# Performance work log

Hardware: AMD Instinct MI355X
Metric: run time of the kernel (lower is better)

## Reference

```python
import jax, jax.numpy as jnp
import numpy as np

N_NODES = 50000
N_EDGES = 800000
NFEAT = 128
NHID = 128
NCLASS = 10
N_GRAPHS = 256


def _segment_mean(vals, idx, num):
    # scatter-mean: sum then divide by count, count clamped to 1 (PyG 'mean' semantics)
    s = jax.ops.segment_sum(vals, idx, num_segments=num)
    c = jax.ops.segment_sum(jnp.ones((vals.shape[0], 1), vals.dtype), idx, num_segments=num)
    return s / jnp.maximum(c, 1.0)


def _graph_conv(x, src, dst, W_n, b_n, W_s):
    # gather x at source nodes, scatter-mean into destination nodes
    agg = _segment_mean(x[src], dst, x.shape[0])          # [N, C_in]
    return agg @ W_n.T + b_n + x @ W_s.T                  # [N, C_out]


def setup_inputs() -> dict:
    key = jax.random.key(0)
    ks = jax.random.split(key, 12)

    def lin_w(k, o, i):
        return (jax.random.uniform(k, (o, i), jnp.float32) * 2.0 - 1.0) / np.sqrt(i)

    x = jax.random.normal(ks[0], (N_NODES, NFEAT), jnp.float32)
    edge_index = jax.random.randint(ks[1], (2, N_EDGES), 0, N_NODES, dtype=jnp.int32)
    batch = jnp.sort(jax.random.randint(ks[2], (N_NODES,), 0, N_GRAPHS, dtype=jnp.int32))

    return {
        "x": x,
        "edge_index": edge_index,
        "batch": batch,
        "W1n": lin_w(ks[3], NHID, NFEAT), "b1": jnp.zeros((NHID,), jnp.float32), "W1s": lin_w(ks[4], NHID, NFEAT),
        "W2n": lin_w(ks[5], NHID, NHID), "b2": jnp.zeros((NHID,), jnp.float32), "W2s": lin_w(ks[6], NHID, NHID),
        "W3n": lin_w(ks[7], NHID, NHID), "b3": jnp.zeros((NHID,), jnp.float32), "W3s": lin_w(ks[8], NHID, NHID),
        "Wlin": lin_w(ks[9], NCLASS, NHID), "blin": jnp.zeros((NCLASS,), jnp.float32),
    }


def reference(x, edge_index, batch, W1n, b1, W1s, W2n, b2, W2s, W3n, b3, W3s, Wlin, blin):
    src, dst = edge_index[0], edge_index[1]
    h = jax.nn.relu(_graph_conv(x, src, dst, W1n, b1, W1s))
    h = jax.nn.relu(_graph_conv(h, src, dst, W2n, b2, W2s))
    h = jax.nn.relu(_graph_conv(h, src, dst, W3n, b3, W3s))
    g = _segment_mean(h, batch, N_GRAPHS)                 # global_mean_pool -> [G, NHID]
    # dropout is identity at inference
    logits = g @ Wlin.T + blin                            # [G, NCLASS]
    return jax.nn.log_softmax(logits, axis=1)
```

## Files before the change

kernel.cpp:

```cpp
#include <hip/hip_runtime.h>
#include <hip/hip_bf16.h>

#define NNODES 50000
#define NEDGES 800000
#define NFEAT 128
#define NHID 128
#define NCLASS 10
#define NGRAPHS 256

#define NB 391
#define HB 512

typedef __attribute__((ext_vector_type(8))) short short8;
typedef __attribute__((ext_vector_type(4))) short short4v;
typedef __attribute__((ext_vector_type(4))) float floatx4;

__device__ __forceinline__ float bf2f(unsigned short u) {
    union { unsigned i; float f; } c; c.i = ((unsigned)u) << 16; return c.f;
}
__device__ __forceinline__ unsigned short f2bf(float f) {
    union { float f; unsigned i; } c; c.f = f;
    unsigned x = c.i;
    unsigned r = (x + 0x7fffu + ((x >> 16) & 1u)) >> 16;
    return (unsigned short)r;
}
__device__ __forceinline__ float blo(unsigned v) { return bf2f((unsigned short)(v & 0xffffu)); }
__device__ __forceinline__ float bhi(unsigned v) { return bf2f((unsigned short)(v >> 16)); }

__device__ __forceinline__ void gload_lds16(const void* gsrc, void* ldst) {
    __builtin_amdgcn_global_load_lds(
        (const __attribute__((address_space(1))) void*)gsrc,
        (__attribute__((address_space(3))) void*)ldst, 16, 0, 0);
}

__global__ __launch_bounds__(256) void k_hist(const int* __restrict__ dst,
                                              int* __restrict__ hist) {
    __shared__ int lh[NB];
    int tid = threadIdx.x;
    for (int b = tid; b < NB; b += 256) lh[b] = 0;
    __syncthreads();
    for (int i = blockIdx.x * 256 + tid; i < NEDGES; i += HB * 256)
        atomicAdd(&lh[dst[i] >> 7], 1);
    __syncthreads();
    for (int b = tid; b < NB; b += 256) hist[b * HB + blockIdx.x] = lh[b];
}

__global__ __launch_bounds__(256) void k_scanA(const int* __restrict__ hist,
                                               int* __restrict__ base,
                                               int* __restrict__ tot) {
    int q = blockIdx.x;
    int tid = threadIdx.x;
    int w = tid >> 6, l = tid & 63;
    int v0 = hist[q * HB + 2 * tid];
    int v1 = hist[q * HB + 2 * tid + 1];
    int s = v0 + v1;
    int ps = s;
    #pragma unroll
    for (int d = 1; d < 64; d <<= 1) { int y = __shfl_up(ps, d); if (l >= d) ps += y; }
    __shared__ int wsum[4];
    if (l == 63) wsum[w] = ps;
    __syncthreads();
    int wbase = 0;
    #pragma unroll
    for (int k = 0; k < 4; ++k) wbase += (k < w) ? wsum[k] : 0;
    int excl = wbase + ps - s;
    base[q * HB + 2 * tid] = excl;
    base[q * HB + 2 * tid + 1] = excl + v0;
    if (tid == 255) tot[q] = wbase + ps;
}

__global__ __launch_bounds__(512) void k_scanB(const int* __restrict__ tot,
                                               int* __restrict__ boff,
                                               int* __restrict__ row_ptr,
                                               const int* __restrict__ batch,
                                               int* __restrict__ gstart) {
    int tid = threadIdx.x;
    int wid = tid >> 6, l = tid & 63;
    if (tid <= NGRAPHS) {
        int lo = 0, hi = NNODES;
        while (lo < hi) { int mid = (lo + hi) >> 1; if (batch[mid] < tid) lo = mid + 1; else hi = mid; }
        gstart[tid] = lo;
    }
    if (wid == 0) {
        int carry = 0;
        #pragma unroll
        for (int c = 0; c < (NB + 63) / 64; ++c) {
            int i = c * 64 + l;
            int v = (i < NB) ? tot[i] : 0;
            int s = v;
            #pragma unroll
            for (int d = 1; d < 64; d <<= 1) { int y = __shfl_up(s, d); if (l >= d) s += y; }
            if (i < NB) boff[i] = carry + s - v;
            carry += __shfl(s, 63);
        }
        if (l == 0) { boff[NB] = carry; row_ptr[NNODES] = carry; }
    }
}

__global__ __launch_bounds__(256) void k_scatter(const int* __restrict__ src,
                                                 const int* __restrict__ dst,
                                                 const int* __restrict__ base,
                                                 const int* __restrict__ boff,
                                                 unsigned* __restrict__ ebuf) {
    __shared__ int cur[NB];
    int tid = threadIdx.x;
    for (int b = tid; b < NB; b += 256) cur[b] = boff[b] + base[b * HB + blockIdx.x];
    __syncthreads();
    for (int i = blockIdx.x * 256 + tid; i < NEDGES; i += HB * 256) {
        int d = dst[i];
        int bin = d >> 7;
        int pos = atomicAdd(&cur[bin], 1);
        ebuf[pos] = (unsigned)src[i] | ((unsigned)(d & 127) << 16);
    }
}

__global__ __launch_bounds__(256) void k_bcsr(const unsigned* __restrict__ ebuf,
                                              const int* __restrict__ boff,
                                              int* __restrict__ row_ptr,
                                              unsigned short* __restrict__ esrc) {
    __shared__ int deg[128];
    __shared__ int curs[128];
    int tid = threadIdx.x;
    int b = blockIdx.x;
    int s = boff[b], e = boff[b + 1];
    if (tid < 128) deg[tid] = 0;
    __syncthreads();
    for (int i = s + tid; i < e; i += 256) atomicAdd(&deg[ebuf[i] >> 16], 1);
    __syncthreads();
    if (tid == 0) {
        int run = s;
        for (int i = 0; i < 128; ++i) { curs[i] = run; run += deg[i]; }
    }
    __syncthreads();
    if (tid < 128) {
        int node = b * 128 + tid;
        if (node < NNODES) row_ptr[node] = curs[tid];
    }
    __syncthreads();
    for (int i = s + tid; i < e; i += 256) {
        unsigned pk = ebuf[i];
        int pos = atomicAdd(&curs[pk >> 16], 1);
        esrc[pos] = (unsigned short)(pk & 0xffffu);
    }
}

__global__ void k_cvt(const float* __restrict__ x,
                      const float* __restrict__ w0, const float* __restrict__ w1,
                      const float* __restrict__ w2, const float* __restrict__ w3,
                      const float* __restrict__ w4, const float* __restrict__ w5,
                      unsigned short* __restrict__ xb, unsigned short* __restrict__ wb) {
    int gid = blockIdx.x * blockDim.x + threadIdx.x;
    const int NX4 = NNODES * NFEAT / 4;
    const floatx4* srcv;
    short4v* dstv;
    if (gid < NX4) {
        srcv = (const floatx4*)x + gid;
        dstv = (short4v*)xb + gid;
    } else {
        int j = gid - NX4;
        if (j >= 6 * 4096) return;
        int m = j >> 12;
        int o4 = j & 4095;
        const float* w = (m == 0) ? w0 : (m == 1) ? w1 : (m == 2) ? w2
                       : (m == 3) ? w3 : (m == 4) ? w4 : w5;
        srcv = (const floatx4*)w + o4;
        dstv = (short4v*)wb + (m * 4096 + o4);
    }
    floatx4 v = *srcv;
    short4v o;
    #pragma unroll
    for (int k = 0; k < 4; ++k) o[k] = (short)f2bf(v[k]);
    *dstv = o;
}

__global__ __launch_bounds__(512, 6) void k_layer(const unsigned short* __restrict__ feat,
                                                  const int* __restrict__ row_ptr,
                                                  const unsigned short* __restrict__ esrc,
                                                  const unsigned short* __restrict__ Bn,
                                                  const unsigned short* __restrict__ Bs,
                                                  const float* __restrict__ bias,
                                                  unsigned short* __restrict__ out) {
    __shared__ __align__(16) unsigned short ldsA[2][8192];
    int w = threadIdx.x >> 6;
    int l = threadIdx.x & 63;
    int r = l & 15;
    int gk = l >> 4;
    int m0 = blockIdx.x * 64;

    {
        int c = l & 15;
        #pragma unroll
        for (int is = 0; is < 2; ++is) {
            int row = is * 32 + (w << 2) + (l >> 4);
            int nrow = m0 + row; if (nrow >= NNODES) nrow = NNODES - 1;
            gload_lds16(feat + (size_t)nrow * 128 + ((c ^ (row & 15)) << 3),
                        &ldsA[1][(is * 32 + (w << 2)) * 128]);
        }
    }

    const unsigned* feat32 = (const unsigned*)feat;
    unsigned* A1 = (unsigned*)&ldsA[0][0];
    #pragma unroll 1
    for (int i = 0; i < 8; ++i) {
        int row = (w << 3) + i;
        int n = m0 + row;
        float a0 = 0.f, a1 = 0.f;
        int nb = 0;
        if (n < NNODES) {
            int beg = row_ptr[n];
            nb = row_ptr[n + 1] - beg;
            for (int base = 0; base < nb; base += 64) {
                int rem = nb - base;
                int cnt = rem < 64 ? rem : 64;
                int myidx = (l < cnt) ? (int)esrc[beg + base + l] : 0;
                int j = 0;
                for (; j + 8 <= cnt; j += 8) {
                    int s0 = __shfl(myidx, j);
                    int s1 = __shfl(myidx, j + 1);
                    int s2 = __shfl(myidx, j + 2);
                    int s3 = __shfl(myidx, j + 3);
                    int s4 = __shfl(myidx, j + 4);
                    int s5 = __shfl(myidx, j + 5);
                    int s6 = __shfl(myidx, j + 6);
                    int s7 = __shfl(myidx, j + 7);
                    unsigned v0 = feat32[s0 * 64 + l];
                    unsigned v1 = feat32[s1 * 64 + l];
                    unsigned v2 = feat32[s2 * 64 + l];
                    unsigned v3 = feat32[s3 * 64 + l];
                    unsigned v4 = feat32[s4 * 64 + l];
                    unsigned v5 = feat32[s5 * 64 + l];
                    unsigned v6 = feat32[s6 * 64 + l];
                    unsigned v7 = feat32[s7 * 64 + l];
                    a0 += ((blo(v0) + blo(v1)) + (blo(v2) + blo(v3)))
                        + ((blo(v4) + blo(v5)) + (blo(v6) + blo(v7)));
                    a1 += ((bhi(v0) + bhi(v1)) + (bhi(v2) + bhi(v3)))
                        + ((bhi(v4) + bhi(v5)) + (bhi(v6) + bhi(v7)));
                }
                for (; j + 4 <= cnt; j += 4) {
                    int s0 = __shfl(myidx, j);
                    int s1 = __shfl(myidx, j + 1);
                    int s2 = __shfl(myidx, j + 2);
                    int s3 = __shfl(myidx, j + 3);
                    unsigned v0 = feat32[s0 * 64 + l];
                    unsigned v1 = feat32[s1 * 64 + l];
                    unsigned v2 = feat32[s2 * 64 + l];
                    unsigned v3 = feat32[s3 * 64 + l];
                    a0 += (blo(v0) + blo(v1)) + (blo(v2) + blo(v3));
                    a1 += (bhi(v0) + bhi(v1)) + (bhi(v2) + bhi(v3));
                }
                for (; j < cnt; ++j) {
                    int s0 = __shfl(myidx, j);
                    unsigned v0 = feat32[s0 * 64 + l];
                    a0 += blo(v0);
                    a1 += bhi(v0);
                }
            }
        }
        float inv = 1.0f / (float)max(nb, 1);
        unsigned o = ((unsigned)f2bf(a0 * inv)) | (((unsigned)f2bf(a1 * inv)) << 16);
        int c = l >> 2;
        A1[row * 64 + ((c ^ (row & 15)) << 2) + (l & 3)] = o;
    }

    short8 bf[8];
    #pragma unroll
    for (int kt = 0; kt < 8; ++kt) {
        const unsigned short* Bbase = (kt < 4 ? Bn : Bs);
        bf[kt] = *(const short8*)(Bbase + (w * 16 + r) * 128 + (kt & 3) * 32 + gk * 8);
    }
    int o = w * 16 + r;
    float bias_v = bias[o];

    __syncthreads();

    #pragma unroll
    for (int t = 0; t < 4; ++t) {
        floatx4 acc = {0.f, 0.f, 0.f, 0.f};
        #pragma unroll
        for (int half = 0; half < 2; ++half) {
            short8 af[4];
            #pragma unroll
            for (int kk = 0; kk < 4; ++kk) {
                int Cr = (((kk << 2) + gk) ^ r) << 3;
                af[kk] = *(const short8*)(&ldsA[half][(t * 16 + r) * 128 + Cr]);
            }
            #pragma unroll
            for (int kk = 0; kk < 4; ++kk)
                acc = __builtin_amdgcn_mfma_f32_16x16x32_bf16(af[kk], bf[half * 4 + kk], acc, 0, 0, 0);
        }
        #pragma unroll
        for (int j = 0; j < 4; ++j) {
            int mrow = m0 + t * 16 + gk * 4 + j;
            if (mrow < NNODES) {
                float v = acc[j] + bias_v;
                v = v > 0.f ? v : 0.f;
                out[mrow * 128 + o] = f2bf(v);
            }
        }
    }
}

__global__ __launch_bounds__(256) void k_pool(const unsigned short* __restrict__ h,
                                              const int* __restrict__ gstart,
                                              float* __restrict__ part) {
    int g = blockIdx.x >> 3;
    int c = blockIdx.x & 7;
    int s = gstart[g], e = gstart[g + 1];
    int len = e - s;
    int cs = s + (len * c) / 8;
    int ce = s + (len * (c + 1)) / 8;
    int w = threadIdx.x >> 6;
    int l = threadIdx.x & 63;
    const unsigned* h32 = (const unsigned*)h;
    float a0 = 0.f, a1 = 0.f;
    for (int n = cs + w; n < ce; n += 4) {
        unsigned v = h32[n * 64 + l];
        a0 += blo(v);
        a1 += bhi(v);
    }
    __shared__ float red[4][128];
    red[w][2 * l] = a0;
    red[w][2 * l + 1] = a1;
    __syncthreads();
    if (w == 0) {
        float r0 = (red[0][2 * l] + red[1][2 * l]) + (red[2][2 * l] + red[3][2 * l]);
        float r1 = (red[0][2 * l + 1] + red[1][2 * l + 1]) + (red[2][2 * l + 1] + red[3][2 * l + 1]);
        float* dst = part + (size_t)(g * 8 + c) * 128;
        dst[2 * l] = r0;
        dst[2 * l + 1] = r1;
    }
}

__global__ __launch_bounds__(128) void k_head(const float* __restrict__ part,
                                              const int* __restrict__ gstart,
                                              const float* __restrict__ Wlin,
                                              const float* __restrict__ blin,
                                              float* __restrict__ out) {
    int gi = blockIdx.x;
    __shared__ float gl[128];
    __shared__ float lg[NCLASS];
    int t = threadIdx.x;
    float s = 0.f;
    #pragma unroll
    for (int c = 0; c < 8; ++c) s += part[(size_t)(gi * 8 + c) * 128 + t];
    int len = gstart[gi + 1] - gstart[gi];
    gl[t] = s / (float)max(len, 1);
    __syncthreads();
    if (t < NCLASS) {
        float a = blin[t];
        #pragma unroll 16
        for (int i = 0; i < 128; ++i) a += gl[i] * Wlin[t * 128 + i];
        lg[t] = a;
    }
    __syncthreads();
    if (t == 0) {
        float m = lg[0];
        for (int k = 1; k < NCLASS; ++k) m = fmaxf(m, lg[k]);
        float sum = 0.f;
        for (int k = 0; k < NCLASS; ++k) sum += expf(lg[k] - m);
        float ls = logf(sum) + m;
        for (int k = 0; k < NCLASS; ++k) out[gi * NCLASS + k] = lg[k] - ls;
    }
}

extern "C" void kernel_launch(void* const* d_in, const int* in_sizes, int n_in,
                              void* d_out, int out_size, void* d_ws, size_t ws_size,
                              hipStream_t stream) {
    const float* x    = (const float*)d_in[0];
    const int*   ei   = (const int*)d_in[1];
    const int*   src  = ei;
    const int*   dst  = ei + NEDGES;
    const int*   batch= (const int*)d_in[2];
    const float* W1n  = (const float*)d_in[3];
    const float* b1   = (const float*)d_in[4];
    const float* W1s  = (const float*)d_in[5];
    const float* W2n  = (const float*)d_in[6];
    const float* b2   = (const float*)d_in[7];
    const float* W2s  = (const float*)d_in[8];
    const float* W3n  = (const float*)d_in[9];
    const float* b3   = (const float*)d_in[10];
    const float* W3s  = (const float*)d_in[11];
    const float* Wlin = (const float*)d_in[12];
    const float* blin = (const float*)d_in[13];
    float* out = (float*)d_out;

    char* p = (char*)d_ws;
    auto alloc = [&](size_t bytes) -> void* {
        void* r = (void*)p;
        p += (bytes + 255) & ~(size_t)255;
        return r;
    };
    unsigned short* xb   = (unsigned short*)alloc((size_t)NNODES * NFEAT * 2);
    unsigned short* hA   = (unsigned short*)alloc((size_t)NNODES * NHID * 2);
    unsigned short* hB   = (unsigned short*)alloc((size_t)NNODES * NHID * 2);
    unsigned short* wb   = (unsigned short*)alloc((size_t)6 * 16384 * 2);
    int* hist    = (int*)alloc((size_t)NB * HB * 4);
    int* base    = (int*)alloc((size_t)NB * HB * 4);
    int* tot     = (int*)alloc((size_t)NB * 4);
    int* boff    = (int*)alloc((size_t)(NB + 1) * 4);
    int* row_ptr = (int*)alloc((size_t)(NNODES + 1) * 4);
    int* gstart  = (int*)alloc((size_t)(NGRAPHS + 1) * 4);
    unsigned* ebuf = (unsigned*)alloc((size_t)NEDGES * 4);
    unsigned short* esrc = (unsigned short*)alloc((size_t)NEDGES * 2);
    float* part  = (float*)alloc((size_t)NGRAPHS * 8 * NHID * 4);

    k_hist<<<HB, 256, 0, stream>>>(dst, hist);
    k_scanA<<<NB, 256, 0, stream>>>(hist, base, tot);
    k_scanB<<<1, 512, 0, stream>>>(tot, boff, row_ptr, batch, gstart);
    k_scatter<<<HB, 256, 0, stream>>>(src, dst, base, boff, ebuf);
    k_bcsr<<<NB, 256, 0, stream>>>(ebuf, boff, row_ptr, esrc);

    {
        int total4 = NNODES * NFEAT / 4 + 6 * 4096;
        k_cvt<<<(total4 + 255) / 256, 256, 0, stream>>>(x, W1n, W1s, W2n, W2s, W3n, W3s, xb, wb);
    }

    const int layerGrid = (NNODES + 63) / 64;

    k_layer<<<layerGrid, 512, 0, stream>>>(xb, row_ptr, esrc, wb + 0 * 16384, wb + 1 * 16384, b1, hA);
    k_layer<<<layerGrid, 512, 0, stream>>>(hA, row_ptr, esrc, wb + 2 * 16384, wb + 3 * 16384, b2, hB);
    k_layer<<<layerGrid, 512, 0, stream>>>(hB, row_ptr, esrc, wb + 4 * 16384, wb + 5 * 16384, b3, hA);

    k_pool<<<NGRAPHS * 8, 256, 0, stream>>>(hA, gstart, part);
    k_head<<<NGRAPHS, 128, 0, stream>>>(part, gstart, Wlin, blin, out);
}
```

Baseline: 170.2 us.

## Fuse histogram with conversion, prefetch row indices in layer, merge pool and head

Merges the edge histogram kernel with the fp32-to-bf16 conversion kernel into one launch, and merges global mean pooling with the classifier head into one kernel per graph. In the layer kernel, each wave loads its 9 row_ptr entries once and prefetches the next node's neighbor indices while aggregating the current one. The aim is fewer launches and lower gather latency, at the cost of pooling running on only 256 blocks instead of 2048.

Result: no change. 172.8 us (+1.6%).

```diff
diff --git a/kernel.cpp b/kernel.cpp
--- a/kernel.cpp
+++ b/kernel.cpp
@@ -33,123 +33,26 @@
         (__attribute__((address_space(3))) void*)ldst, 16, 0, 0);
 }
 
-__global__ __launch_bounds__(256) void k_hist(const int* __restrict__ dst,
-                                              int* __restrict__ hist) {
-    __shared__ int lh[NB];
+__global__ __launch_bounds__(256) void k_histcvt(const int* __restrict__ dst,
+                                                 int* __restrict__ hist,
+                                                 const float* __restrict__ x,
+                                                 const float* __restrict__ w0, const float* __restrict__ w1,
+                                                 const float* __restrict__ w2, const float* __restrict__ w3,
+                                                 const float* __restrict__ w4, const float* __restrict__ w5,
+                                                 unsigned short* __restrict__ xb,
+                                                 unsigned short* __restrict__ wb) {
     int tid = threadIdx.x;
-    for (int b = tid; b < NB; b += 256) lh[b] = 0;
-    __syncthreads();
-    for (int i = blockIdx.x * 256 + tid; i < NEDGES; i += HB * 256)
-        atomicAdd(&lh[dst[i] >> 7], 1);
-    __syncthreads();
-    for (int b = tid; b < NB; b += 256) hist[b * HB + blockIdx.x] = lh[b];
-}
-
-__global__ __launch_bounds__(256) void k_scanA(const int* __restrict__ hist,
-                                               int* __restrict__ base,
-                                               int* __restrict__ tot) {
-    int q = blockIdx.x;
-    int tid = threadIdx.x;
-    int w = tid >> 6, l = tid & 63;
-    int v0 = hist[q * HB + 2 * tid];
-    int v1 = hist[q * HB + 2 * tid + 1];
-    int s = v0 + v1;
-    int ps = s;
-    #pragma unroll
-    for (int d = 1; d < 64; d <<= 1) { int y = __shfl_up(ps, d); if (l >= d) ps += y; }
-    __shared__ int wsum[4];
-    if (l == 63) wsum[w] = ps;
-    __syncthreads();
-    int wbase = 0;
-    #pragma unroll
-    for (int k = 0; k < 4; ++k) wbase += (k < w) ? wsum[k] : 0;
-    int excl = wbase + ps - s;
-    base[q * HB + 2 * tid] = excl;
-    base[q * HB + 2 * tid + 1] = excl + v0;
-    if (tid == 255) tot[q] = wbase + ps;
-}
-
-__global__ __launch_bounds__(512) void k_scanB(const int* __restrict__ tot,
-                                               int* __restrict__ boff,
-                                               int* __restrict__ row_ptr,
-                                               const int* __restrict__ batch,
-                                               int* __restrict__ gstart) {
-    int tid = threadIdx.x;
-    int wid = tid >> 6, l = tid & 63;
-    if (tid <= NGRAPHS) {
-        int lo = 0, hi = NNODES;
-        while (lo < hi) { int mid = (lo + hi) >> 1; if (batch[mid] < tid) lo = mid + 1; else hi = mid; }
-        gstart[tid] = lo;
-    }
-    if (wid == 0) {
-        int carry = 0;
-        #pragma unroll
-        for (int c = 0; c < (NB + 63) / 64; ++c) {
-            int i = c * 64 + l;
-            int v = (i < NB) ? tot[i] : 0;
-            int s = v;
-            #pragma unroll
-            for (int d = 1; d < 64; d <<= 1) { int y = __shfl_up(s, d); if (l >= d) s += y; }
-            if (i < NB) boff[i] = carry + s - v;
-            carry += __shfl(s, 63);
-        }
-        if (l == 0) { boff[NB] = carry; row_ptr[NNODES] = carry; }
-    }
-}
-
-__global__ __launch_bounds__(256) void k_scatter(const int* __restrict__ src,
-                                                 const int* __restrict__ dst,
-                                                 const int* __restrict__ base,
-                                                 const int* __restrict__ boff,
-                                                 unsigned* __restrict__ ebuf) {
-    __shared__ int cur[NB];
-    int tid = threadIdx.x;
-    for (int b = tid; b < NB; b += 256) cur[b] = boff[b] + base[b * HB + blockIdx.x];
-    __syncthreads();
-    for (int i = blockIdx.x * 256 + tid; i < NEDGES; i += HB * 256) {
-        int d = dst[i];
-        int bin = d >> 7;
-        int pos = atomicAdd(&cur[bin], 1);
-        ebuf[pos] = (unsigned)src[i] | ((unsigned)(d & 127) << 16);
-    }
-}
-
-__global__ __launch_bounds__(256) void k_bcsr(const unsigned* __restrict__ ebuf,
-                                              const int* __restrict__ boff,
-                                              int* __restrict__ row_ptr,
-                                              unsigned short* __restrict__ esrc) {
-    __shared__ int deg[128];
-    __shared__ int curs[128];
-    int tid = threadIdx.x;
-    int b = blockIdx.x;
-    int s = boff[b], e = boff[b + 1];
-    if (tid < 128) deg[tid] = 0;
-    __syncthreads();
-    for (int i = s + tid; i < e; i += 256) atomicAdd(&deg[ebuf[i] >> 16], 1);
-    __syncthreads();
-    if (tid == 0) {
-        int run = s;
-        for (int i = 0; i < 128; ++i) { curs[i] = run; run += deg[i]; }
-    }
-    __syncthreads();
-    if (tid < 128) {
-        int node = b * 128 + tid;
-        if (node < NNODES) row_ptr[node] = curs[tid];
-    }
-    __syncthreads();
-    for (int i = s + tid; i < e; i += 256) {
-        unsigned pk = ebuf[i];
-        int pos = atomicAdd(&curs[pk >> 16], 1);
-        esrc[pos] = (unsigned short)(pk & 0xffffu);
-    }
-}
-
-__global__ void k_cvt(const float* __restrict__ x,
-                      const float* __restrict__ w0, const float* __restrict__ w1,
-                      const float* __restrict__ w2, const float* __restrict__ w3,
-                      const float* __restrict__ w4, const float* __restrict__ w5,
-                      unsigned short* __restrict__ xb, unsigned short* __restrict__ wb) {
-    int gid = blockIdx.x * blockDim.x + threadIdx.x;
+    if (blockIdx.x < HB) {
+        __shared__ int lh[NB];
+        for (int b = tid; b < NB; b += 256) lh[b] = 0;
+        __syncthreads();
+        for (int i = blockIdx.x * 256 + tid; i < NEDGES; i += HB * 256)
+            atomicAdd(&lh[dst[i] >> 7], 1);
+        __syncthreads();
+        for (int b = tid; b < NB; b += 256) hist[b * HB + blockIdx.x] = lh[b];
+        return;
+    }
+    int gid = (blockIdx.x - HB) * 256 + tid;
     const int NX4 = NNODES * NFEAT / 4;
     const floatx4* srcv;
     short4v* dstv;
@@ -173,6 +76,105 @@
     *dstv = o;
 }
 
+__global__ __launch_bounds__(256) void k_scanA(const int* __restrict__ hist,
+                                               int* __restrict__ base,
+                                               int* __restrict__ tot) {
+    int q = blockIdx.x;
+    int tid = threadIdx.x;
+    int w = tid >> 6, l = tid & 63;
+    int v0 = hist[q * HB + 2 * tid];
+    int v1 = hist[q * HB + 2 * tid + 1];
+    int s = v0 + v1;
+    int ps = s;
+    #pragma unroll
+    for (int d = 1; d < 64; d <<= 1) { int y = __shfl_up(ps, d); if (l >= d) ps += y; }
+    __shared__ int wsum[4];
+    if (l == 63) wsum[w] = ps;
+    __syncthreads();
+    int wbase = 0;
+    #pragma unroll
+    for (int k = 0; k < 4; ++k) wbase += (k < w) ? wsum[k] : 0;
+    int excl = wbase + ps - s;
+    base[q * HB + 2 * tid] = excl;
+    base[q * HB + 2 * tid + 1] = excl + v0;
+    if (tid == 255) tot[q] = wbase + ps;
+}
+
+__global__ __launch_bounds__(512) void k_scanB(const int* __restrict__ tot,
+                                               int* __restrict__ boff,
+                                               int* __restrict__ row_ptr,
+                                               const int* __restrict__ batch,
+                                               int* __restrict__ gstart) {
+    int tid = threadIdx.x;
+    int wid = tid >> 6, l = tid & 63;
+    if (tid <= NGRAPHS) {
+        int lo = 0, hi = NNODES;
+        while (lo < hi) { int mid = (lo + hi) >> 1; if (batch[mid] < tid) lo = mid + 1; else hi = mid; }
+        gstart[tid] = lo;
+    }
+    if (wid == 0) {
+        int carry = 0;
+        #pragma unroll
+        for (int c = 0; c < (NB + 63) / 64; ++c) {
+            int i = c * 64 + l;
+            int v = (i < NB) ? tot[i] : 0;
+            int s = v;
+            #pragma unroll
+            for (int d = 1; d < 64; d <<= 1) { int y = __shfl_up(s, d); if (l >= d) s += y; }
+            if (i < NB) boff[i] = carry + s - v;
+            carry += __shfl(s, 63);
+        }
+        if (l == 0) { boff[NB] = carry; row_ptr[NNODES] = carry; }
+    }
+}
+
+__global__ __launch_bounds__(256) void k_scatter(const int* __restrict__ src,
+                                                 const int* __restrict__ dst,
+                                                 const int* __restrict__ base,
+                                                 const int* __restrict__ boff,
+                                                 unsigned* __restrict__ ebuf) {
+    __shared__ int cur[NB];
+    int tid = threadIdx.x;
+    for (int b = tid; b < NB; b += 256) cur[b] = boff[b] + base[b * HB + blockIdx.x];
+    __syncthreads();
+    for (int i = blockIdx.x * 256 + tid; i < NEDGES; i += HB * 256) {
+        int d = dst[i];
+        int bin = d >> 7;
+        int pos = atomicAdd(&cur[bin], 1);
+        ebuf[pos] = (unsigned)src[i] | ((unsigned)(d & 127) << 16);
+    }
+}
+
+__global__ __launch_bounds__(256) void k_bcsr(const unsigned* __restrict__ ebuf,
+                                              const int* __restrict__ boff,
+                                              int* __restrict__ row_ptr,
+                                              unsigned short* __restrict__ esrc) {
+    __shared__ int deg[128];
+    __shared__ int curs[128];
+    int tid = threadIdx.x;
+    int b = blockIdx.x;
+    int s = boff[b], e = boff[b + 1];
+    if (tid < 128) deg[tid] = 0;
+    __syncthreads();
+    for (int i = s + tid; i < e; i += 256) atomicAdd(&deg[ebuf[i] >> 16], 1);
+    __syncthreads();
+    if (tid == 0) {
+        int run = s;
+        for (int i = 0; i < 128; ++i) { curs[i] = run; run += deg[i]; }
+    }
+    __syncthreads();
+    if (tid < 128) {
+        int node = b * 128 + tid;
+        if (node < NNODES) row_ptr[node] = curs[tid];
+    }
+    __syncthreads();
+    for (int i = s + tid; i < e; i += 256) {
+        unsigned pk = ebuf[i];
+        int pos = atomicAdd(&curs[pk >> 16], 1);
+        esrc[pos] = (unsigned short)(pk & 0xffffu);
+    }
+}
+
 __global__ __launch_bounds__(512, 6) void k_layer(const unsigned short* __restrict__ feat,
                                                   const int* __restrict__ row_ptr,
                                                   const unsigned short* __restrict__ esrc,
@@ -200,66 +202,74 @@
 
     const unsigned* feat32 = (const unsigned*)feat;
     unsigned* A1 = (unsigned*)&ldsA[0][0];
+    int n0 = m0 + (w << 3);
+    int rpl = row_ptr[min(n0 + l, NNODES)];
+    int beg = __shfl(rpl, 0);
+    int nb  = __shfl(rpl, 1) - beg;
+    int myidx = (l < (nb < 64 ? nb : 64)) ? (int)esrc[beg + l] : 0;
+
     #pragma unroll 1
     for (int i = 0; i < 8; ++i) {
+        int nbeg = 0, nnb = 0, nmy = 0;
+        if (i < 7) {
+            nbeg = __shfl(rpl, i + 1);
+            nnb  = __shfl(rpl, i + 2) - nbeg;
+            nmy  = (l < (nnb < 64 ? nnb : 64)) ? (int)esrc[nbeg + l] : 0;
+        }
+        float a0 = 0.f, a1 = 0.f;
+        for (int base = 0; base < nb; base += 64) {
+            int rem = nb - base;
+            int cnt = rem < 64 ? rem : 64;
+            int idxv = (base == 0) ? myidx
+                     : ((l < cnt) ? (int)esrc[beg + base + l] : 0);
+            int j = 0;
+            for (; j + 8 <= cnt; j += 8) {
+                int s0 = __shfl(idxv, j);
+                int s1 = __shfl(idxv, j + 1);
+                int s2 = __shfl(idxv, j + 2);
+                int s3 = __shfl(idxv, j + 3);
+                int s4 = __shfl(idxv, j + 4);
+                int s5 = __shfl(idxv, j + 5);
+                int s6 = __shfl(idxv, j + 6);
+                int s7 = __shfl(idxv, j + 7);
+                unsigned v0 = feat32[s0 * 64 + l];
+                unsigned v1 = feat32[s1 * 64 + l];
+                unsigned v2 = feat32[s2 * 64 + l];
+                unsigned v3 = feat32[s3 * 64 + l];
+                unsigned v4 = feat32[s4 * 64 + l];
+                unsigned v5 = feat32[s5 * 64 + l];
+                unsigned v6 = feat32[s6 * 64 + l];
+                unsigned v7 = feat32[s7 * 64 + l];
+                a0 += ((blo(v0) + blo(v1)) + (blo(v2) + blo(v3)))
+                    + ((blo(v4) + blo(v5)) + (blo(v6) + blo(v7)));
+                a1 += ((bhi(v0) + bhi(v1)) + (bhi(v2) + bhi(v3)))
+                    + ((bhi(v4) + bhi(v5)) + (bhi(v6) + bhi(v7)));
+            }
+            for (; j + 4 <= cnt; j += 4) {
+                int s0 = __shfl(idxv, j);
+                int s1 = __shfl(idxv, j + 1);
+                int s2 = __shfl(idxv, j + 2);
+                int s3 = __shfl(idxv, j + 3);
+                unsigned v0 = feat32[s0 * 64 + l];
+                unsigned v1 = feat32[s1 * 64 + l];
+                unsigned v2 = feat32[s2 * 64 + l];
+                unsigned v3 = feat32[s3 * 64 + l];
+                a0 += (blo(v0) + blo(v1)) + (blo(v2) + blo(v3));
+                a1 += (bhi(v0) + bhi(v1)) + (bhi(v2) + bhi(v3));
+            }
+            for (; j < cnt; ++j) {
+                int s0 = __shfl(idxv, j);
+                unsigned v0 = feat32[s0 * 64 + l];
+                a0 += blo(v0);
+                a1 += bhi(v0);
+            }
+        }
         int row = (w << 3) + i;
-        int n = m0 + row;
-        float a0 = 0.f, a1 = 0.f;
-        int nb = 0;
-        if (n < NNODES) {
-            int beg = row_ptr[n];
-            nb = row_ptr[n + 1] - beg;
-            for (int base = 0; base < nb; base += 64) {
-                int rem = nb - base;
-                int cnt = rem < 64 ? rem : 64;
-                int myidx = (l < cnt) ? (int)esrc[beg + base + l] : 0;
-                int j = 0;
-                for (; j + 8 <= cnt; j += 8) {
-                    int s0 = __shfl(myidx, j);
-                    int s1 = __shfl(myidx, j + 1);
-                    int s2 = __shfl(myidx, j + 2);
-                    int s3 = __shfl(myidx, j + 3);
-                    int s4 = __shfl(myidx, j + 4);
-                    int s5 = __shfl(myidx, j + 5);
-                    int s6 = __shfl(myidx, j + 6);
-                    int s7 = __shfl(myidx, j + 7);
-                    unsigned v0 = feat32[s0 * 64 + l];
-                    unsigned v1 = feat32[s1 * 64 + l];
-                    unsigned v2 = feat32[s2 * 64 + l];
-                    unsigned v3 = feat32[s3 * 64 + l];
-                    unsigned v4 = feat32[s4 * 64 + l];
-                    unsigned v5 = feat32[s5 * 64 + l];
-                    unsigned v6 = feat32[s6 * 64 + l];
-                    unsigned v7 = feat32[s7 * 64 + l];
-                    a0 += ((blo(v0) + blo(v1)) + (blo(v2) + blo(v3)))
-                        + ((blo(v4) + blo(v5)) + (blo(v6) + blo(v7)));
-                    a1 += ((bhi(v0) + bhi(v1)) + (bhi(v2) + bhi(v3)))
-                        + ((bhi(v4) + bhi(v5)) + (bhi(v6) + bhi(v7)));
-                }
-                for (; j + 4 <= cnt; j += 4) {
-                    int s0 = __shfl(myidx, j);
-                    int s1 = __shfl(myidx, j + 1);
-                    int s2 = __shfl(myidx, j + 2);
-                    int s3 = __shfl(myidx, j + 3);
-                    unsigned v0 = feat32[s0 * 64 + l];
-                    unsigned v1 = feat32[s1 * 64 + l];
-                    unsigned v2 = feat32[s2 * 64 + l];
-                    unsigned v3 = feat32[s3 * 64 + l];
-                    a0 += (blo(v0) + blo(v1)) + (blo(v2) + blo(v3));
-                    a1 += (bhi(v0) + bhi(v1)) + (bhi(v2) + bhi(v3));
-                }
-                for (; j < cnt; ++j) {
-                    int s0 = __shfl(myidx, j);
-                    unsigned v0 = feat32[s0 * 64 + l];
-                    a0 += blo(v0);
-                    a1 += bhi(v0);
-                }
-            }
-        }
         float inv = 1.0f / (float)max(nb, 1);
         unsigned o = ((unsigned)f2bf(a0 * inv)) | (((unsigned)f2bf(a1 * inv)) << 16);
         int c = l >> 2;
         A1[row * 64 + ((c ^ (row & 15)) << 2) + (l & 3)] = o;
+        beg = nbeg; nb = nnb; myidx = nmy;
     }
 
     short8 bf[8];
@@ -300,51 +310,32 @@
     }
 }
 
-__global__ __launch_bounds__(256) void k_pool(const unsigned short* __restrict__ h,
-                                              const int* __restrict__ gstart,
-                                              float* __restrict__ part) {
-    int g = blockIdx.x >> 3;
-    int c = blockIdx.x & 7;
-    int s = gstart[g], e = gstart[g + 1];
-    int len = e - s;
-    int cs = s + (len * c) / 8;
-    int ce = s + (len * (c + 1)) / 8;
+__global__ __launch_bounds__(256) void k_poolhead(const unsigned short* __restrict__ h,
+                                                  const int* __restrict__ gstart,
+                                                  const float* __restrict__ Wlin,
+                                                  const float* __restrict__ blin,
+                                                  float* __restrict__ out) {
+    int gi = blockIdx.x;
     int w = threadIdx.x >> 6;
     int l = threadIdx.x & 63;
+    int t = threadIdx.x;
+    int s = gstart[gi], e = gstart[gi + 1];
     const unsigned* h32 = (const unsigned*)h;
     float a0 = 0.f, a1 = 0.f;
-    for (int n = cs + w; n < ce; n += 4) {
+    for (int n = s + w; n < e; n += 4) {
         unsigned v = h32[n * 64 + l];
         a0 += blo(v);
         a1 += bhi(v);
     }
     __shared__ float red[4][128];
+    __shared__ float gl[128];
+    __shared__ float lg[NCLASS];
     red[w][2 * l] = a0;
     red[w][2 * l + 1] = a1;
     __syncthreads();
-    if (w == 0) {
-        float r0 = (red[0][2 * l] + red[1][2 * l]) + (red[2][2 * l] + red[3][2 * l]);
-        float r1 = (red[0][2 * l + 1] + red[1][2 * l + 1]) + (red[2][2 * l + 1] + red[3][2 * l + 1]);
-        float* dst = part + (size_t)(g * 8 + c) * 128;
-        dst[2 * l] = r0;
-        dst[2 * l + 1] = r1;
-    }
-}
-
-__global__ __launch_bounds__(128) void k_head(const float* __restrict__ part,
-                                              const int* __restrict__ gstart,
-                                              const float* __restrict__ Wlin,
-                                              const float* __restrict__ blin,
-                                              float* __restrict__ out) {
-    int gi = blockIdx.x;
-    __shared__ float gl[128];
-    __shared__ float lg[NCLASS];
-    int t = threadIdx.x;
-    float s = 0.f;
-    #pragma unroll
-    for (int c = 0; c < 8; ++c) s += part[(size_t)(gi * 8 + c) * 128 + t];
-    int len = gstart[gi + 1] - gstart[gi];
-    gl[t] = s / (float)max(len, 1);
+    float invlen = 1.0f / (float)max(e - s, 1);
+    if (t < 128)
+        gl[t] = ((red[0][t] + red[1][t]) + (red[2][t] + red[3][t])) * invlen;
     __syncthreads();
     if (t < NCLASS) {
         float a = blin[t];
@@ -402,25 +393,22 @@
     int* gstart  = (int*)alloc((size_t)(NGRAPHS + 1) * 4);
     unsigned* ebuf = (unsigned*)alloc((size_t)NEDGES * 4);
     unsigned short* esrc = (unsigned short*)alloc((size_t)NEDGES * 2);
-    float* part  = (float*)alloc((size_t)NGRAPHS * 8 * NHID * 4);
-
-    k_hist<<<HB, 256, 0, stream>>>(dst, hist);
+
+    {
+        int cvtBlocks = (NNODES * NFEAT / 4 + 6 * 4096 + 255) / 256;
+        k_histcvt<<<HB + cvtBlocks, 256, 0, stream>>>(dst, hist, x,
+                                                      W1n, W1s, W2n, W2s, W3n, W3s, xb, wb);
+    }
     k_scanA<<<NB, 256, 0, stream>>>(hist, base, tot);
     k_scanB<<<1, 512, 0, stream>>>(tot, boff, row_ptr, batch, gstart);
     k_scatter<<<HB, 256, 0, stream>>>(src, dst, base, boff, ebuf);
     k_bcsr<<<NB, 256, 0, stream>>>(ebuf, boff, row_ptr, esrc);
 
-    {
-        int total4 = NNODES * NFEAT / 4 + 6 * 4096;
-        k_cvt<<<(total4 + 255) / 256, 256, 0, stream>>>(x, W1n, W1s, W2n, W2s, W3n, W3s, xb, wb);
-    }
-
     const int layerGrid = (NNODES + 63) / 64;
 
     k_layer<<<layerGrid, 512, 0, stream>>>(xb, row_ptr, esrc, wb + 0 * 16384, wb + 1 * 16384, b1, hA);
     k_layer<<<layerGrid, 512, 0, stream>>>(hA, row_ptr, esrc, wb + 2 * 16384, wb + 3 * 16384, b2, hB);
     k_layer<<<layerGrid, 512, 0, stream>>>(hB, row_ptr, esrc, wb + 4 * 16384, wb + 5 * 16384, b3, hA);
 
-    k_pool<<<NGRAPHS * 8, 256, 0, stream>>>(hA, gstart, part);
-    k_head<<<NGRAPHS, 128, 0, stream>>>(part, gstart, Wlin, blin, out);
-}
+    k_poolhead<<<NGRAPHS, 256, 0, stream>>>(hA, gstart, Wlin, blin, out);
+}
```
